# Kernel optimization log

Hardware: AMD Instinct MI355X
Metric: run time of the kernel (lower is better)

The kernel has to match this reference:

```python
import jax, jax.numpy as jnp
import numpy as np

VOCAB = 100000
SEQ = 2048
NSYN = 4
D = 300      # embedding_size
H1 = 300     # biLSTM output dim (150 per direction)
U = 150      # LSTM units per direction


def _lstm(x, Wk, Wr, b, reverse=False):
    """Keras-style LSTM over [S, D] -> [S, U]. Gate order i, f, g(cell), o."""
    if reverse:
        x = x[::-1]
    u = Wr.shape[0]

    def step(carry, xt):
        h, c = carry
        z = xt @ Wk + h @ Wr + b              # [4U]
        i, f, g, o = jnp.split(z, 4, axis=-1)
        i = jax.nn.sigmoid(i)
        f = jax.nn.sigmoid(f)
        g = jnp.tanh(g)
        o = jax.nn.sigmoid(o)
        c = f * c + i * g
        h = o * jnp.tanh(c)
        return (h, c), h

    init = (jnp.zeros((u,), x.dtype), jnp.zeros((u,), x.dtype))
    _, hs = jax.lax.scan(step, init, x)
    return hs[::-1] if reverse else hs


def setup_inputs() -> dict:
    key = jax.random.key(0)
    ks = jax.random.split(key, 14)
    w = 0.05  # small init so exp() attention coefficients stay stable
    return {
        "sentence": jax.random.randint(ks[0], (SEQ,), 0, VOCAB),
        "synonym_indices": jax.random.randint(ks[1], (VOCAB, NSYN), 0, VOCAB),
        "embedding_matrix": jax.random.normal(ks[2], (VOCAB, D), jnp.float32) * 0.1,
        # forward LSTM
        "Wk_f": jax.random.normal(ks[3], (D, 4 * U), jnp.float32) * w,
        "Wr_f": jax.random.normal(ks[4], (U, 4 * U), jnp.float32) * w,
        "b_f": jnp.zeros((4 * U,), jnp.float32),
        # backward LSTM
        "Wk_b": jax.random.normal(ks[5], (D, 4 * U), jnp.float32) * w,
        "Wr_b": jax.random.normal(ks[6], (U, 4 * U), jnp.float32) * w,
        "b_b": jnp.zeros((4 * U,), jnp.float32),
        # primary attention dense (h1 -> h1)
        "W1": jax.random.normal(ks[7], (H1, H1), jnp.float32) * w,
        "b1": jnp.zeros((H1,), jnp.float32),
        # secondary attention dense (h1 -> 1, tanh)
        "W2": jax.random.normal(ks[8], (H1, 1), jnp.float32) * w,
        "b2": jnp.zeros((1,), jnp.float32),
        # output heads
        "We": jax.random.normal(ks[9], (H1, 8), jnp.float32) * w,
        "be": jnp.zeros((8,), jnp.float32),
        "Ws": jax.random.normal(ks[10], (H1, 1), jnp.float32) * w,
        "bs": jnp.zeros((1,), jnp.float32),
    }


def reference(sentence, synonym_indices, embedding_matrix,
              Wk_f, Wr_f, b_f, Wk_b, Wr_b, b_b,
              W1, b1, W2, b2, We, be, Ws, bs):
    emb = embedding_matrix[sentence]                       # [S, D]
    hf = _lstm(emb, Wk_f, Wr_f, b_f)                       # [S, U]
    hb = _lstm(emb, Wk_b, Wr_b, b_b, reverse=True)         # [S, U]
    hidden = jnp.concatenate([hf, hb], axis=-1)            # [S, H1]

    # ---- primary attention (vectorized over all tokens) ----
    out = hidden @ W1 + b1                                 # [S, H1]
    S = sentence.shape[0]
    # Faithful off-by-one from the original loop: token 0 uses row 0,
    # token i (i>=1) uses out/hidden row i-1.
    idx = jnp.concatenate([jnp.zeros((1,), jnp.int32),
                           jnp.arange(S - 1, dtype=jnp.int32)])
    syn_emb = embedding_matrix[synonym_indices[sentence]]  # [S, NSYN, D]
    coeff = jnp.exp(jnp.einsum('skd,sd->sk', syn_emb, out[idx]))  # [S, NSYN]
    m = jnp.einsum('sk,skd->sd', coeff, syn_emb)           # [S, D]
    h_hats = m + hidden[idx]                               # [S, H1]

    # ---- secondary attention ----
    c2 = jnp.exp(jnp.tanh(h_hats @ W2 + b2))               # [S, 1]
    H = jnp.sum(c2 * h_hats, axis=0)[None, :]              # [1, H1]

    emotion_logits = H @ We + be                           # [1, 8]
    sentiment_logits = H @ Ws + bs                         # [1, 1]
    return (emotion_logits, sentiment_logits)
```

## Files before the change

kernel.cpp:

```cpp
#include <hip/hip_runtime.h>
#include <hip/hip_bf16.h>

#define SEQ   2048
#define DIM   300
#define UU    150
#define G4    600
#define H1    300
#define NSYN  4

typedef _Float16 half2v __attribute__((ext_vector_type(2)));
typedef unsigned u32x4 __attribute__((ext_vector_type(4)));
union HU { unsigned u; half2v h; };

static __device__ __forceinline__ float sigm(float x) { return 1.0f / (1.0f + __expf(-x)); }
static __device__ __forceinline__ float tanh_fast(float x) { return 1.0f - 2.0f / (1.0f + __expf(2.0f * x)); }

static __device__ __forceinline__ float dot2v(unsigned w, unsigned h, float acc) {
    asm("v_dot2_f32_f16 %0, %1, %2, %0" : "+v"(acc) : "v"(w), "v"(h));
    return acc;
}

#define LDS_BARRIER() asm volatile("s_waitcnt lgkmcnt(0)\n\ts_barrier" ::: "memory")

__global__ void xpre_kernel(const int* __restrict__ sentence,
                            const float* __restrict__ emb_mat,
                            const float* __restrict__ Wk_f,
                            const float* __restrict__ b_f,
                            const float* __restrict__ Wk_b,
                            const float* __restrict__ b_b,
                            float* __restrict__ Xf, float* __restrict__ Xb)
{
    const int dir = blockIdx.y;
    const float* Wk = dir ? Wk_b : Wk_f;
    const float* bb = dir ? b_b : b_f;
    float* X = dir ? Xb : Xf;

    const int s0  = blockIdx.x * 8;
    const int tid = threadIdx.x;

    __shared__ int   sids[8];
    __shared__ float embs[8][DIM];

    if (tid < 8) sids[tid] = sentence[s0 + tid];
    __syncthreads();
    for (int e = tid; e < 8 * DIM; e += 640) {
        int r = e / DIM, d = e - r * DIM;
        embs[r][d] = emb_mat[(long)sids[r] * DIM + d];
    }
    __syncthreads();

    if (tid < G4) {
        float acc[8];
        float bv = bb[tid];
        #pragma unroll
        for (int r = 0; r < 8; ++r) acc[r] = bv;
        for (int k = 0; k < DIM; ++k) {
            float wv = Wk[k * G4 + tid];
            #pragma unroll
            for (int r = 0; r < 8; ++r) acc[r] = fmaf(embs[r][k], wv, acc[r]);
        }
        #pragma unroll
        for (int r = 0; r < 8; ++r) X[(long)(s0 + r) * G4 + tid] = acc[r];
    }
}

#define REP76(F) \
  F(0) F(1) F(2) F(3) F(4) F(5) F(6) F(7) F(8) F(9) \
  F(10) F(11) F(12) F(13) F(14) F(15) F(16) F(17) F(18) F(19) \
  F(20) F(21) F(22) F(23) F(24) F(25) F(26) F(27) F(28) F(29) \
  F(30) F(31) F(32) F(33) F(34) F(35) F(36) F(37) F(38) F(39) \
  F(40) F(41) F(42) F(43) F(44) F(45) F(46) F(47) F(48) F(49) \
  F(50) F(51) F(52) F(53) F(54) F(55) F(56) F(57) F(58) F(59) \
  F(60) F(61) F(62) F(63) F(64) F(65) F(66) F(67) F(68) F(69) \
  F(70) F(71) F(72) F(73) F(74) F(75)

static __device__ __forceinline__ unsigned packpair2(const float* __restrict__ Wr, int c, int k) {
    if (k >= 75) return 0u;
    HU x;
    x.h.x = (_Float16)Wr[(2 * k) * G4 + c];
    x.h.y = (_Float16)Wr[(2 * k + 1) * G4 + c];
    return x.u;
}

__global__ __launch_bounds__(640)
void lstm_scan_kernel(
    const float* __restrict__ Xf, const float* __restrict__ Xb,
    const float* __restrict__ Wr_f, const float* __restrict__ Wr_b,
    float* __restrict__ hidden)
{
    const int dir = blockIdx.x;
    const float* X  = dir ? Xb : Xf;
    const float* Wr = dir ? Wr_b : Wr_f;
    const int tid = threadIdx.x;
    const int g   = tid & 3;
    const int q   = tid >> 2;
    const bool active = (q < UU);
    const int u   = active ? q : (UU - 1);
    const int col = g * UU + u;

    __shared__ __align__(16) unsigned hsbuf[2][80];

#define WDECL(k) unsigned w_##k;
    REP76(WDECL)
#undef WDECL
#define WLOAD(k) w_##k = packpair2(Wr, col, k);
    REP76(WLOAD)
#undef WLOAD

    for (int e = tid; e < 160; e += 640) ((unsigned*)hsbuf)[e] = 0u;

    float c = 0.0f;
    int tt = dir ? (SEQ - 1) : 0;
    const int dt = dir ? -1 : 1;
    float x = X[(long)tt * G4 + col];
    const bool writer = (g == 1) && active;
    float* hout = hidden + dir * UU + u;
    __syncthreads();

    for (int step = 0; step < SEQ; ++step) {
        const int tn = (step < SEQ - 1) ? (tt + dt) : tt;
        float xn = X[(long)tn * G4 + col];

        const u32x4* hb = (const u32x4*)hsbuf[step & 1];
        u32x4 h0 = hb[0], h1 = hb[1], h2 = hb[2], h3 = hb[3], h4 = hb[4];

        float aa = x, ab = 0.0f;

#define DOTQ(k0,k1,k2,k3,hv) \
        aa = dot2v(w_##k0, hv.x, aa); ab = dot2v(w_##k1, hv.y, ab); \
        aa = dot2v(w_##k2, hv.z, aa); ab = dot2v(w_##k3, hv.w, ab);

        DOTQ(0,1,2,3,h0)     DOTQ(4,5,6,7,h1)     DOTQ(8,9,10,11,h2)
        DOTQ(12,13,14,15,h3) DOTQ(16,17,18,19,h4)
        h0 = hb[5]; h1 = hb[6]; h2 = hb[7]; h3 = hb[8]; h4 = hb[9];
        DOTQ(20,21,22,23,h0) DOTQ(24,25,26,27,h1) DOTQ(28,29,30,31,h2)
        DOTQ(32,33,34,35,h3) DOTQ(36,37,38,39,h4)
        h0 = hb[10]; h1 = hb[11]; h2 = hb[12]; h3 = hb[13]; h4 = hb[14];
        DOTQ(40,41,42,43,h0) DOTQ(44,45,46,47,h1) DOTQ(48,49,50,51,h2)
        DOTQ(52,53,54,55,h3) DOTQ(56,57,58,59,h4)
        h0 = hb[15]; h1 = hb[16]; h2 = hb[17]; h3 = hb[18];
        DOTQ(60,61,62,63,h0) DOTQ(64,65,66,67,h1) DOTQ(68,69,70,71,h2)
        DOTQ(72,73,74,75,h3)
#undef DOTQ

        const float z = aa + ab;

        float s  = sigm(z);
        float tz = tanh_fast(z);
        float act  = (g == 2) ? tz : s;
        float act2 = __shfl_xor(act, 2);
        float p    = act * act2;
        float px   = __shfl_xor(p, 1);
        c = s * c + px;
        float th = tanh_fast(c);
        float hv = act2 * th;

        if (writer) {
            ((_Float16*)hsbuf[(step & 1) ^ 1])[u] = (_Float16)hv;
            hout[(long)tt * H1] = hv;
        }
        LDS_BARRIER();

        x = xn; tt = tn;
    }
}

__global__ void w1_kernel(const float* __restrict__ hidden,
                          const float* __restrict__ W1,
                          const float* __restrict__ b1,
                          float* __restrict__ outm)
{
    const int s0  = blockIdx.x * 8;
    const int tid = threadIdx.x;
    __shared__ float hl[8][H1];
    for (int e = tid; e < 8 * H1; e += 320)
        hl[e / H1][e - (e / H1) * H1] = hidden[(long)s0 * H1 + e];
    __syncthreads();

    if (tid < H1) {
        float acc[8];
        float bv = b1[tid];
        #pragma unroll
        for (int r = 0; r < 8; ++r) acc[r] = bv;
        for (int k = 0; k < H1; ++k) {
            float wv = W1[k * H1 + tid];
            #pragma unroll
            for (int r = 0; r < 8; ++r) acc[r] = fmaf(hl[r][k], wv, acc[r]);
        }
        #pragma unroll
        for (int r = 0; r < 8; ++r) outm[(long)(s0 + r) * H1 + tid] = acc[r];
    }
}

static __device__ __forceinline__ float4 blockReduce4(float4 v, float* red, int tid)
{
    #pragma unroll
    for (int off = 32; off > 0; off >>= 1) {
        v.x += __shfl_down(v.x, off);
        v.y += __shfl_down(v.y, off);
        v.z += __shfl_down(v.z, off);
        v.w += __shfl_down(v.w, off);
    }
    __syncthreads();
    if ((tid & 63) == 0) {
        int wv = tid >> 6;
        red[wv * 4 + 0] = v.x; red[wv * 4 + 1] = v.y;
        red[wv * 4 + 2] = v.z; red[wv * 4 + 3] = v.w;
    }
    __syncthreads();
    float4 r;
    r.x = red[0]; r.y = red[1]; r.z = red[2]; r.w = red[3];
    #pragma unroll
    for (int wv = 1; wv < 5; ++wv) {
        r.x += red[wv * 4 + 0]; r.y += red[wv * 4 + 1];
        r.z += red[wv * 4 + 2]; r.w += red[wv * 4 + 3];
    }
    return r;
}

static __device__ __forceinline__ float blockReduce1(float v, float* red, int tid)
{
    #pragma unroll
    for (int off = 32; off > 0; off >>= 1) v += __shfl_down(v, off);
    __syncthreads();
    if ((tid & 63) == 0) red[tid >> 6] = v;
    __syncthreads();
    return red[0] + red[1] + red[2] + red[3] + red[4];
}

__global__ void attn_kernel(const int* __restrict__ sentence,
                            const int* __restrict__ syn_idx,
                            const float* __restrict__ emb_mat,
                            const float* __restrict__ outm,
                            const float* __restrict__ hidden,
                            const float* __restrict__ W2,
                            const float* __restrict__ b2,
                            float* __restrict__ whh)
{
    const int s   = blockIdx.x;
    const int t   = s ? (s - 1) : 0;
    const int tid = threadIdx.x;
    __shared__ float red[20];

    const int sent = sentence[s];
    const long i0 = (long)syn_idx[sent * NSYN + 0] * DIM;
    const long i1 = (long)syn_idx[sent * NSYN + 1] * DIM;
    const long i2 = (long)syn_idx[sent * NSYN + 2] * DIM;
    const long i3 = (long)syn_idx[sent * NSYN + 3] * DIM;

    float se0 = 0.f, se1 = 0.f, se2 = 0.f, se3 = 0.f, od = 0.f, hd = 0.f;
    if (tid < DIM) {
        se0 = emb_mat[i0 + tid];
        se1 = emb_mat[i1 + tid];
        se2 = emb_mat[i2 + tid];
        se3 = emb_mat[i3 + tid];
        od  = outm[(long)t * H1 + tid];
        hd  = hidden[(long)t * H1 + tid];
    }

    float4 dots = blockReduce4(make_float4(se0 * od, se1 * od, se2 * od, se3 * od), red, tid);
    float c0 = __expf(dots.x), c1 = __expf(dots.y), c2c = __expf(dots.z), c3 = __expf(dots.w);

    float hh = fmaf(c0, se0, fmaf(c1, se1, fmaf(c2c, se2, fmaf(c3, se3, hd))));

    float w2v = (tid < DIM) ? W2[tid] : 0.f;
    float dot2 = blockReduce1(hh * w2v, red, tid);
    float cc = __expf(tanh_fast(dot2 + b2[0]));

    if (tid < DIM) whh[(long)s * H1 + tid] = cc * hh;
}

__global__ void hred_kernel(const float* __restrict__ whh, float* __restrict__ H)
{
    const int d   = blockIdx.x;
    const int tid = threadIdx.x;
    float acc = 0.f;
    for (int s = tid; s < SEQ; s += 256) acc += whh[(long)s * H1 + d];
    #pragma unroll
    for (int off = 32; off > 0; off >>= 1) acc += __shfl_down(acc, off);
    __shared__ float red[4];
    if ((tid & 63) == 0) red[tid >> 6] = acc;
    __syncthreads();
    if (tid == 0) H[d] = red[0] + red[1] + red[2] + red[3];
}

__global__ void logits_kernel(const float* __restrict__ H,
                              const float* __restrict__ We,
                              const float* __restrict__ be,
                              const float* __restrict__ Ws,
                              const float* __restrict__ bs,
                              float* __restrict__ outp)
{
    const int e = threadIdx.x;
    if (e < 9) {
        float acc = (e < 8) ? be[e] : bs[0];
        for (int d = 0; d < H1; ++d) {
            float wv = (e < 8) ? We[d * 8 + e] : Ws[d];
            acc = fmaf(H[d], wv, acc);
        }
        outp[e] = acc;
    }
}

extern "C" void kernel_launch(void* const* d_in, const int* in_sizes, int n_in,
                              void* d_out, int out_size, void* d_ws, size_t ws_size,
                              hipStream_t stream)
{
    const int* sentence   = (const int*)d_in[0];
    const int* syn_idx    = (const int*)d_in[1];
    const float* emb      = (const float*)d_in[2];
    const float* Wk_f     = (const float*)d_in[3];
    const float* Wr_f     = (const float*)d_in[4];
    const float* b_f      = (const float*)d_in[5];
    const float* Wk_b     = (const float*)d_in[6];
    const float* Wr_b     = (const float*)d_in[7];
    const float* b_b      = (const float*)d_in[8];
    const float* W1       = (const float*)d_in[9];
    const float* b1       = (const float*)d_in[10];
    const float* W2       = (const float*)d_in[11];
    const float* b2       = (const float*)d_in[12];
    const float* We       = (const float*)d_in[13];
    const float* be       = (const float*)d_in[14];
    const float* Ws       = (const float*)d_in[15];
    const float* bs       = (const float*)d_in[16];

    float* ws     = (float*)d_ws;
    float* Xf     = ws;
    float* Xb     = Xf + (long)SEQ * G4;
    float* hidden = Xb + (long)SEQ * G4;
    float* outm   = hidden + (long)SEQ * H1;
    float* whh    = outm + (long)SEQ * H1;
    float* H      = whh + (long)SEQ * H1;

    float* outp = (float*)d_out;

    xpre_kernel<<<dim3(SEQ / 8, 2), 640, 0, stream>>>(sentence, emb, Wk_f, b_f, Wk_b, b_b, Xf, Xb);
    lstm_scan_kernel<<<2, 640, 0, stream>>>(Xf, Xb, Wr_f, Wr_b, hidden);
    w1_kernel<<<SEQ / 8, 320, 0, stream>>>(hidden, W1, b1, outm);
    attn_kernel<<<SEQ, 320, 0, stream>>>(sentence, syn_idx, emb, outm, hidden, W2, b2, whh);
    hred_kernel<<<H1, 256, 0, stream>>>(whh, H);
    logits_kernel<<<1, 64, 0, stream>>>(H, We, be, Ws, bs, outp);
}
```

Measured before the change: 2.428 ms.

## Move LSTM recurrent weights from registers to LDS via a pre-pack kernel

```diff
diff --git a/kernel.cpp b/kernel.cpp
--- a/kernel.cpp
+++ b/kernel.cpp
@@ -7,6 +7,8 @@
 #define G4    600
 #define H1    300
 #define NSYN  4
+#define NGRP  19
+#define NLDS  16
 
 typedef _Float16 half2v __attribute__((ext_vector_type(2)));
 typedef unsigned u32x4 __attribute__((ext_vector_type(4)));
@@ -64,49 +66,54 @@
     }
 }
 
-#define REP76(F) \
-  F(0) F(1) F(2) F(3) F(4) F(5) F(6) F(7) F(8) F(9) \
-  F(10) F(11) F(12) F(13) F(14) F(15) F(16) F(17) F(18) F(19) \
-  F(20) F(21) F(22) F(23) F(24) F(25) F(26) F(27) F(28) F(29) \
-  F(30) F(31) F(32) F(33) F(34) F(35) F(36) F(37) F(38) F(39) \
-  F(40) F(41) F(42) F(43) F(44) F(45) F(46) F(47) F(48) F(49) \
-  F(50) F(51) F(52) F(53) F(54) F(55) F(56) F(57) F(58) F(59) \
-  F(60) F(61) F(62) F(63) F(64) F(65) F(66) F(67) F(68) F(69) \
-  F(70) F(71) F(72) F(73) F(74) F(75)
-
-static __device__ __forceinline__ unsigned packpair2(const float* __restrict__ Wr, int c, int k) {
-    if (k >= 75) return 0u;
-    HU x;
-    x.h.x = (_Float16)Wr[(2 * k) * G4 + c];
-    x.h.y = (_Float16)Wr[(2 * k + 1) * G4 + c];
-    return x.u;
+__global__ void pack_kernel(const float* __restrict__ Wr_f,
+                            const float* __restrict__ Wr_b,
+                            unsigned* __restrict__ pw)
+{
+    const int kc  = blockIdx.x;
+    const int dir = blockIdx.y;
+    const int t   = threadIdx.x;
+    if (t >= G4) return;
+    const float* Wr = dir ? Wr_b : Wr_f;
+    const int c = (t & 3) * UU + (t >> 2);
+
+    unsigned out[4];
+    #pragma unroll
+    for (int j = 0; j < 4; ++j) {
+        int p  = 4 * kc + j;
+        int r0 = 2 * p, r1 = 2 * p + 1;
+        float a = (r0 < UU) ? Wr[r0 * G4 + c] : 0.0f;
+        float b = (r1 < UU) ? Wr[r1 * G4 + c] : 0.0f;
+        HU x; x.h.x = (_Float16)a; x.h.y = (_Float16)b;
+        out[j] = x.u;
+    }
+    u32x4* dst = (u32x4*)(pw + (((long)dir * NGRP + kc) * G4 + t) * 4);
+    u32x4 v; v.x = out[0]; v.y = out[1]; v.z = out[2]; v.w = out[3];
+    *dst = v;
 }
 
 __global__ __launch_bounds__(640)
 void lstm_scan_kernel(
     const float* __restrict__ Xf, const float* __restrict__ Xb,
-    const float* __restrict__ Wr_f, const float* __restrict__ Wr_b,
+    const unsigned* __restrict__ pw,
     float* __restrict__ hidden)
 {
     const int dir = blockIdx.x;
-    const float* X  = dir ? Xb : Xf;
-    const float* Wr = dir ? Wr_b : Wr_f;
+    const float* X = dir ? Xb : Xf;
+    const u32x4* pwd = (const u32x4*)pw + (long)dir * NGRP * G4;
+
     const int tid = threadIdx.x;
     const int g   = tid & 3;
     const int q   = tid >> 2;
     const bool active = (q < UU);
     const int u   = active ? q : (UU - 1);
     const int col = g * UU + u;
-
+    const int lcol = active ? tid : (596 + g);
+
+    __shared__ u32x4 wlds[NLDS * G4];
     __shared__ __align__(16) unsigned hsbuf[2][80];
 
-#define WDECL(k) unsigned w_##k;
-    REP76(WDECL)
-#undef WDECL
-#define WLOAD(k) w_##k = packpair2(Wr, col, k);
-    REP76(WLOAD)
-#undef WLOAD
-
+    for (int e = tid; e < NLDS * G4; e += 640) wlds[e] = pwd[e];
     for (int e = tid; e < 160; e += 640) ((unsigned*)hsbuf)[e] = 0u;
 
     float c = 0.0f;
@@ -115,33 +122,37 @@
     float x = X[(long)tt * G4 + col];
     const bool writer = (g == 1) && active;
     float* hout = hidden + dir * UU + u;
+    const u32x4* wthr = wlds + lcol;
+    const u32x4* gthr = pwd + NLDS * G4 + lcol;
     __syncthreads();
 
     for (int step = 0; step < SEQ; ++step) {
         const int tn = (step < SEQ - 1) ? (tt + dt) : tt;
         float xn = X[(long)tn * G4 + col];
+        u32x4 wg0 = gthr[0 * G4];
+        u32x4 wg1 = gthr[1 * G4];
+        u32x4 wg2 = gthr[2 * G4];
 
         const u32x4* hb = (const u32x4*)hsbuf[step & 1];
-        u32x4 h0 = hb[0], h1 = hb[1], h2 = hb[2], h3 = hb[3], h4 = hb[4];
 
         float aa = x, ab = 0.0f;
 
-#define DOTQ(k0,k1,k2,k3,hv) \
-        aa = dot2v(w_##k0, hv.x, aa); ab = dot2v(w_##k1, hv.y, ab); \
-        aa = dot2v(w_##k2, hv.z, aa); ab = dot2v(w_##k3, hv.w, ab);
-
-        DOTQ(0,1,2,3,h0)     DOTQ(4,5,6,7,h1)     DOTQ(8,9,10,11,h2)
-        DOTQ(12,13,14,15,h3) DOTQ(16,17,18,19,h4)
-        h0 = hb[5]; h1 = hb[6]; h2 = hb[7]; h3 = hb[8]; h4 = hb[9];
-        DOTQ(20,21,22,23,h0) DOTQ(24,25,26,27,h1) DOTQ(28,29,30,31,h2)
-        DOTQ(32,33,34,35,h3) DOTQ(36,37,38,39,h4)
-        h0 = hb[10]; h1 = hb[11]; h2 = hb[12]; h3 = hb[13]; h4 = hb[14];
-        DOTQ(40,41,42,43,h0) DOTQ(44,45,46,47,h1) DOTQ(48,49,50,51,h2)
-        DOTQ(52,53,54,55,h3) DOTQ(56,57,58,59,h4)
-        h0 = hb[15]; h1 = hb[16]; h2 = hb[17]; h3 = hb[18];
-        DOTQ(60,61,62,63,h0) DOTQ(64,65,66,67,h1) DOTQ(68,69,70,71,h2)
-        DOTQ(72,73,74,75,h3)
-#undef DOTQ
+        #pragma unroll
+        for (int kc = 0; kc < NLDS; ++kc) {
+            u32x4 wv = wthr[kc * G4];
+            u32x4 hv = hb[kc];
+            aa = dot2v(wv.x, hv.x, aa); ab = dot2v(wv.y, hv.y, ab);
+            aa = dot2v(wv.z, hv.z, aa); ab = dot2v(wv.w, hv.w, ab);
+        }
+        { u32x4 hv = hb[16];
+          aa = dot2v(wg0.x, hv.x, aa); ab = dot2v(wg0.y, hv.y, ab);
+          aa = dot2v(wg0.z, hv.z, aa); ab = dot2v(wg0.w, hv.w, ab); }
+        { u32x4 hv = hb[17];
+          aa = dot2v(wg1.x, hv.x, aa); ab = dot2v(wg1.y, hv.y, ab);
+          aa = dot2v(wg1.z, hv.z, aa); ab = dot2v(wg1.w, hv.w, ab); }
+        { u32x4 hv = hb[18];
+          aa = dot2v(wg2.x, hv.x, aa); ab = dot2v(wg2.y, hv.y, ab);
+          aa = dot2v(wg2.z, hv.z, aa); ab = dot2v(wg2.w, hv.w, ab); }
 
         const float z = aa + ab;
 
@@ -331,11 +342,13 @@
     float* outm   = hidden + (long)SEQ * H1;
     float* whh    = outm + (long)SEQ * H1;
     float* H      = whh + (long)SEQ * H1;
+    unsigned* pw  = (unsigned*)(H + H1);
 
     float* outp = (float*)d_out;
 
     xpre_kernel<<<dim3(SEQ / 8, 2), 640, 0, stream>>>(sentence, emb, Wk_f, b_f, Wk_b, b_b, Xf, Xb);
-    lstm_scan_kernel<<<2, 640, 0, stream>>>(Xf, Xb, Wr_f, Wr_b, hidden);
+    pack_kernel<<<dim3(NGRP, 2), 640, 0, stream>>>(Wr_f, Wr_b, pw);
+    lstm_scan_kernel<<<2, 640, 0, stream>>>(Xf, Xb, pw, hidden);
     w1_kernel<<<SEQ / 8, 320, 0, stream>>>(hidden, W1, b1, outm);
     attn_kernel<<<SEQ, 320, 0, stream>>>(sentence, syn_idx, emb, outm, hidden, W2, b2, whh);
     hred_kernel<<<H1, 256, 0, stream>>>(whh, H);
```

New measurement: 2.974 ms. 22.5% more time.
